# Kernel tuning notes

Measured on AMD Instinct MI355X. Metric: run time of the kernel, lower is better.

The kernel has to match this reference:

```python
import jax, jax.numpy as jnp
from jax import lax
import numpy as np

B, DIM, HEADS, H, W = 4, 384, 8, 128, 128


def conv2d(x, w, b, groups=1, pad=0):
    # x: NCHW, w: OIHW (I = in_channels // groups)
    y = lax.conv_general_dilated(
        x, w, window_strides=(1, 1), padding=[(pad, pad), (pad, pad)],
        dimension_numbers=("NCHW", "OIHW", "NCHW"), feature_group_count=groups)
    return y + b[None, :, None, None]


def _l2norm(x, eps=1e-12):
    # torch F.normalize(dim=-1): x / max(||x||_2, eps)
    n = jnp.sqrt(jnp.sum(x * x, axis=-1, keepdims=True))
    return x / jnp.maximum(n, eps)


def setup_inputs() -> dict:
    key = jax.random.key(0)
    ks = jax.random.split(key, 8)
    s = 0.02
    d = DIM
    return {
        "x": jax.random.normal(ks[0], (B, d, H, W), jnp.float32),
        "feature": jax.random.normal(ks[1], (B, d, H, W), jnp.float32),
        "qkv_w": jax.random.normal(ks[2], (3 * d, d, 1, 1), jnp.float32) * s,
        "qkv_b": jnp.zeros((3 * d,), jnp.float32),
        "dw_w": jax.random.normal(ks[3], (3 * d, 1, 3, 3), jnp.float32) * s,  # depthwise, groups=3d
        "dw_b": jnp.zeros((3 * d,), jnp.float32),
        "qdw_w": jax.random.normal(ks[4], (2 * d, 1, 3, 3), jnp.float32) * s,  # depthwise, groups=2d
        "qdw_b": jnp.zeros((2 * d,), jnp.float32),
        "qpw_w": jax.random.normal(ks[5], (d, 2 * d, 1, 1), jnp.float32) * s,
        "qpw_b": jnp.zeros((d,), jnp.float32),
        "proj_w": jax.random.normal(ks[6], (d, d, 1, 1), jnp.float32) * s,
        "proj_b": jnp.zeros((d,), jnp.float32),
        "temperature": jnp.ones((HEADS, 1, 1), jnp.float32),
        "K": 24,  # top-k count == int(C * 0.5) with C = DIM // HEADS = 48
    }


def reference(x, feature, qkv_w, qkv_b, dw_w, dw_b, qdw_w, qdw_b,
              qpw_w, qpw_b, proj_w, proj_b, temperature, K):
    b, c, h, w = x.shape
    # qkv = dwconv3x3(conv1x1(x))
    qkv = conv2d(conv2d(x, qkv_w, qkv_b), dw_w, dw_b, groups=3 * c, pad=1)
    q, k, v = jnp.split(qkv, 3, axis=1)
    # q branch: dwconv3x3 on cat([q, feature]) -> GELU(exact) -> 1x1 conv
    qf = conv2d(jnp.concatenate([q, feature], axis=1), qdw_w, qdw_b, groups=2 * c, pad=1)
    qf = jax.nn.gelu(qf, approximate=False)
    q = conv2d(qf, qpw_w, qpw_b)

    def heads(t):
        return t.reshape(b, HEADS, c // HEADS, h * w)  # b head C (h w)

    q = _l2norm(heads(q))
    k = _l2norm(heads(k))
    v = heads(v)
    # channel attention: [b,head,C,C]
    attn = jnp.einsum("bhcn,bhdn->bhcd", q, k) * temperature
    vals, idx = lax.top_k(attn, K)
    neg = jnp.full_like(attn, -jnp.inf)
    attn = jnp.put_along_axis(neg, idx, vals, axis=-1, inplace=False)
    attn = jax.nn.softmax(attn, axis=-1)
    out = jnp.einsum("bhcd,bhdn->bhcn", attn, v).reshape(b, c, h, w)
    return conv2d(out, proj_w, proj_b)
```

## Files before the change

### kernel.cpp

```cpp
#include <hip/hip_runtime.h>

using u16 = unsigned short;
typedef __attribute__((ext_vector_type(8))) __bf16 bf16x8;
typedef __attribute__((ext_vector_type(4))) float  f32x4;
typedef __attribute__((ext_vector_type(8))) u16    u16x8;
typedef __attribute__((ext_vector_type(4))) u16    u16x4;

#define NB   4
#define DIM  384
#define NPIX 16384

__device__ __forceinline__ u16 f2bf(float f) {
  return __builtin_bit_cast(u16, (__bf16)f);
}
__device__ __forceinline__ float bf2f(u16 u) {
  return (float)__builtin_bit_cast(__bf16, u);
}
__device__ __forceinline__ void gload16(const void* g, void* l) {
  __builtin_amdgcn_global_load_lds(
      (const __attribute__((address_space(1))) void*)g,
      (__attribute__((address_space(3))) void*)l, 16, 0, 0);
}

__global__ void k_cvt(const float* __restrict__ s, u16* __restrict__ d, int n) {
  int i = blockIdx.x * 256 + threadIdx.x;
  if (i < n) d[i] = f2bf(s[i]);
}
__global__ void k_cvt2(const float* __restrict__ s, u16* __restrict__ hi,
                       u16* __restrict__ lo, int n) {
  int i = blockIdx.x * 256 + threadIdx.x;
  if (i < n) {
    float v = s[i];
    u16 h = f2bf(v);
    hi[i] = h;
    lo[i] = f2bf(v - bf2f(h));
  }
}

__global__ void k_splitx(const float* __restrict__ x, u16* __restrict__ xhi,
                         u16* __restrict__ xlo) {
  __shared__ float tile[32][33];
  int n0 = blockIdx.x * 32, c0 = blockIdx.y * 32, b = blockIdx.z;
  int tj = threadIdx.x & 31, ti = threadIdx.x >> 5;
  const float* xp = x + ((size_t)b * DIM + c0) * NPIX + n0;
  #pragma unroll
  for (int i = ti; i < 32; i += 8) tile[i][tj] = xp[(size_t)i * NPIX + tj];
  __syncthreads();
  const size_t ob = ((size_t)b * NPIX + n0) * DIM + c0;
  #pragma unroll
  for (int j = ti; j < 32; j += 8) {
    float v = tile[tj][j];
    u16 h = f2bf(v);
    xhi[ob + (size_t)j * DIM + tj] = h;
    xlo[ob + (size_t)j * DIM + tj] = f2bf(v - bf2f(h));
  }
}

template<int OUTMODE>
__global__ __launch_bounds__(256, 4)
void k_gemmS(const u16* __restrict__ A, const u16* __restrict__ B,
             void* __restrict__ Out, const float* __restrict__ bias,
             int M, int N, int Kd)
{
  __shared__ u16 lA[128 * 64];
  __shared__ u16 lB[128 * 64];
  const int tid = threadIdx.x, wid = tid >> 6, lane = tid & 63;
  const int GX = gridDim.x, GY = gridDim.y;
  const int W = GX * GY * (int)gridDim.z;
  const int w = blockIdx.x + GX * (blockIdx.y + GY * blockIdx.z);
  const int nw = (w & 7) * (W >> 3) + (w >> 3);
  const int mt = nw % GY;
  const int rest = nw / GY;
  const int ntile = rest % GX;
  const int b = rest / GX;
  const int m0 = mt * 128, n0 = ntile * 128;

  const int srow = lane >> 3;
  const int sslot = (lane & 7) ^ srow;
  const size_t rowA = (size_t)(m0 + wid * 32 + srow) * Kd + sslot * 8;
  const size_t rowB = ((size_t)b * N + n0 + wid * 32 + srow) * Kd + sslot * 8;
  u16* lAw = &lA[(wid * 32) * 64];
  u16* lBw = &lB[(wid * 32) * 64];
  const int wm = (wid & 1) * 64, wn = (wid >> 1) * 64;
  const int cl = lane & 15, rl = lane >> 4;
  const int sxa = cl & 7;

  f32x4 acc[4][4];
  const f32x4 fz = {0.f, 0.f, 0.f, 0.f};
  #pragma unroll
  for (int i = 0; i < 4; ++i)
    #pragma unroll
    for (int j = 0; j < 4; ++j) acc[i][j] = fz;

  const int nk = Kd >> 6;
  for (int kt = 0; kt < nk; ++kt) {
    const u16* Ap = A + rowA + kt * 64;
    const u16* Bp = B + rowB + kt * 64;
    __syncthreads();
    #pragma unroll
    for (int i = 0; i < 4; ++i) {
      gload16(Ap + (size_t)(i * 8) * Kd, lAw + i * 8 * 64);
      gload16(Bp + (size_t)(i * 8) * Kd, lBw + i * 8 * 64);
    }
    __syncthreads();
    #pragma unroll
    for (int ks = 0; ks < 2; ++ks) {
      bf16x8 av[4], bv[4];
      #pragma unroll
      for (int i = 0; i < 4; ++i) {
        av[i] = *(const bf16x8*)&lA[(wm + i * 16 + cl) * 64 + ((ks * 4 + rl) ^ sxa) * 8];
        bv[i] = *(const bf16x8*)&lB[(wn + i * 16 + cl) * 64 + ((ks * 4 + rl) ^ sxa) * 8];
      }
      #pragma unroll
      for (int i = 0; i < 4; ++i)
        #pragma unroll
        for (int j = 0; j < 4; ++j)
          acc[i][j] = __builtin_amdgcn_mfma_f32_16x16x32_bf16(av[i], bv[j], acc[i][j], 0, 0, 0);
    }
  }

  #pragma unroll
  for (int i = 0; i < 4; ++i) {
    #pragma unroll
    for (int j = 0; j < 4; ++j) {
      #pragma unroll
      for (int r = 0; r < 4; ++r) {
        const int m = m0 + wm + i * 16 + rl * 4 + r;
        const int n = n0 + wn + j * 16 + cl;
        const float v = acc[i][j][r] + bias[m];
        const size_t o = ((size_t)b * M + m) * N + n;
        if (OUTMODE == 0) ((float*)Out)[o] = v;
        else ((u16*)Out)[o] = f2bf(v);
      }
    }
  }
}

template<int OUTMODE, bool SSQ>
__global__ __launch_bounds__(256, 4)
void k_gemmP(const u16* __restrict__ Ahi, const u16* __restrict__ Alo,
             const u16* __restrict__ Bhi, const u16* __restrict__ Blo,
             void* __restrict__ Out, u16* __restrict__ OutLo,
             const float* __restrict__ bias, float* __restrict__ ssq,
             int M, int N, int Kd)
{
  __shared__ u16 lA[128 * 64];
  __shared__ u16 lB[128 * 64];
  const int tid = threadIdx.x, wid = tid >> 6, lane = tid & 63;
  const int GX = gridDim.x, GY = gridDim.y;
  const int W = GX * GY * (int)gridDim.z;
  const int w = blockIdx.x + GX * (blockIdx.y + GY * blockIdx.z);
  const int nw = (w & 7) * (W >> 3) + (w >> 3);
  const int mt = nw % GY;
  const int rest = nw / GY;
  const int ntile = rest % GX;
  const int b = rest / GX;
  const int m0 = mt * 128, n0 = ntile * 128;

  const int srow = lane >> 3;
  const int sp = (lane & 7) ^ srow;
  const int scol = (sp & 3) * 8;
  const u16* baseA = (sp < 4) ? Ahi : Alo;
  const u16* baseB = (sp < 4) ? Bhi : Blo;
  const u16* srcA[4];
  const u16* srcB[4];
  #pragma unroll
  for (int i = 0; i < 4; ++i) {
    srcA[i] = baseA + (size_t)(m0 + wid * 32 + i * 8 + srow) * Kd + scol;
    srcB[i] = baseB + ((size_t)b * N + n0 + wid * 32 + i * 8 + srow) * Kd + scol;
  }
  u16* lAw = &lA[(wid * 32) * 64];
  u16* lBw = &lB[(wid * 32) * 64];
  const int wm = (wid & 1) * 64, wn = (wid >> 1) * 64;
  const int cl = lane & 15, rl = lane >> 4;
  const int ph = rl ^ (cl & 7);

  f32x4 acc[4][4];
  const f32x4 fz = {0.f, 0.f, 0.f, 0.f};
  #pragma unroll
  for (int i = 0; i < 4; ++i)
    #pragma unroll
    for (int j = 0; j < 4; ++j) acc[i][j] = fz;

  const int nk = Kd >> 5;
  for (int kt = 0; kt < nk; ++kt) {
    __syncthreads();
    #pragma unroll
    for (int i = 0; i < 4; ++i) {
      gload16(srcA[i] + kt * 32, lAw + i * 8 * 64);
      gload16(srcB[i] + kt * 32, lBw + i * 8 * 64);
    }
    __syncthreads();
    bf16x8 avh[4], bvh[4], avl[4], bvl[4];
    #pragma unroll
    for (int i = 0; i < 4; ++i) {
      avh[i] = *(const bf16x8*)&lA[(wm + i * 16 + cl) * 64 + ph * 8];
      bvh[i] = *(const bf16x8*)&lB[(wn + i * 16 + cl) * 64 + ph * 8];
    }
    #pragma unroll
    for (int i = 0; i < 4; ++i)
      #pragma unroll
      for (int j = 0; j < 4; ++j)
        acc[i][j] = __builtin_amdgcn_mfma_f32_16x16x32_bf16(avh[i], bvh[j], acc[i][j], 0, 0, 0);
    #pragma unroll
    for (int i = 0; i < 4; ++i)
      avl[i] = *(const bf16x8*)&lA[(wm + i * 16 + cl) * 64 + (ph ^ 4) * 8];
    #pragma unroll
    for (int i = 0; i < 4; ++i)
      #pragma unroll
      for (int j = 0; j < 4; ++j)
        acc[i][j] = __builtin_amdgcn_mfma_f32_16x16x32_bf16(avl[i], bvh[j], acc[i][j], 0, 0, 0);
    #pragma unroll
    for (int i = 0; i < 4; ++i)
      bvl[i] = *(const bf16x8*)&lB[(wn + i * 16 + cl) * 64 + (ph ^ 4) * 8];
    #pragma unroll
    for (int i = 0; i < 4; ++i)
      #pragma unroll
      for (int j = 0; j < 4; ++j)
        acc[i][j] = __builtin_amdgcn_mfma_f32_16x16x32_bf16(avh[i], bvl[j], acc[i][j], 0, 0, 0);
  }

  float sq[4][4];
  if (SSQ) {
    #pragma unroll
    for (int i = 0; i < 4; ++i)
      #pragma unroll
      for (int r = 0; r < 4; ++r) sq[i][r] = 0.f;
  }
  #pragma unroll
  for (int i = 0; i < 4; ++i) {
    #pragma unroll
    for (int j = 0; j < 4; ++j) {
      #pragma unroll
      for (int r = 0; r < 4; ++r) {
        const int m = m0 + wm + i * 16 + rl * 4 + r;
        const int n = n0 + wn + j * 16 + cl;
        const float v = acc[i][j][r] + bias[m];
        if (SSQ) sq[i][r] += v * v;
        const size_t o = ((size_t)b * M + m) * N + n;
        if (OUTMODE == 0) ((float*)Out)[o] = v;
        else {
          u16 h = f2bf(v);
          ((u16*)Out)[o] = h;
          OutLo[o] = f2bf(v - bf2f(h));
        }
      }
    }
  }
  if (SSQ) {
    #pragma unroll
    for (int i = 0; i < 4; ++i) {
      #pragma unroll
      for (int r = 0; r < 4; ++r) {
        float s = sq[i][r];
        s += __shfl_xor(s, 1);
        s += __shfl_xor(s, 2);
        s += __shfl_xor(s, 4);
        s += __shfl_xor(s, 8);
        if (cl == 0)
          atomicAdd(&ssq[(size_t)b * M + m0 + wm + i * 16 + rl * 4 + r], s);
      }
    }
  }
}

__device__ __forceinline__ void row_acc_f32(const float* __restrict__ rowp,
    int x0, float w0, float w1, float w2,
    float& o0, float& o1, float& o2, float& o3)
{
  float4 r = *(const float4*)(rowp + x0);
  float lm = __shfl_up(r.w, 1);   if (x0 == 0)   lm = 0.f;
  float rt = __shfl_down(r.x, 1); if (x0 == 124) rt = 0.f;
  o0 = fmaf(lm,  w0, fmaf(r.x, w1, fmaf(r.y, w2, o0)));
  o1 = fmaf(r.x, w0, fmaf(r.y, w1, fmaf(r.z, w2, o1)));
  o2 = fmaf(r.y, w0, fmaf(r.z, w1, fmaf(r.w, w2, o2)));
  o3 = fmaf(r.z, w0, fmaf(r.w, w1, fmaf(rt,  w2, o3)));
}
__device__ __forceinline__ void row_acc_bf16(const u16* __restrict__ rowp,
    int x0, float w0, float w1, float w2,
    float& o0, float& o1, float& o2, float& o3)
{
  u16x4 rv = *(const u16x4*)(rowp + x0);
  float r0 = bf2f(rv[0]), r1 = bf2f(rv[1]), r2 = bf2f(rv[2]), r3 = bf2f(rv[3]);
  float lm = __shfl_up(r3, 1);   if (x0 == 0)   lm = 0.f;
  float rt = __shfl_down(r0, 1); if (x0 == 124) rt = 0.f;
  o0 = fmaf(lm, w0, fmaf(r0, w1, fmaf(r1, w2, o0)));
  o1 = fmaf(r0, w0, fmaf(r1, w1, fmaf(r2, w2, o1)));
  o2 = fmaf(r1, w0, fmaf(r2, w1, fmaf(r3, w2, o2)));
  o3 = fmaf(r2, w0, fmaf(r3, w1, fmaf(rt, w2, o3)));
}

__global__ __launch_bounds__(256, 4)
void k_dw3qk(const float* __restrict__ src, const float* __restrict__ w9,
             const float* __restrict__ bias, float* __restrict__ qdwbuf,
             u16* __restrict__ khi, u16* __restrict__ klo,
             float* __restrict__ ssqk)
{
  const int tid = threadIdx.x, wv = tid >> 6, lane = tid & 63;
  const int n0 = blockIdx.x * 1024 + tid * 4;
  const int h = n0 >> 7, x0 = n0 & 127;
  const int c0 = blockIdx.y * 8, b = blockIdx.z;
  const int hm = (h > 0) ? h - 1 : 0, hp = (h < 127) ? h + 1 : 127;
  const float topf = (h > 0) ? 1.f : 0.f, botf = (h < 127) ? 1.f : 0.f;
  const float* base = src + ((size_t)b * 768 + c0) * NPIX;
  const bool isk = (c0 >= 384);
  float ssl[8];
  #pragma unroll
  for (int s = 0; s < 8; ++s) {
    const int c = c0 + s;
    const float* sp = base + (size_t)s * NPIX;
    const float* wc = w9 + c * 9;
    const float bz = bias[c];
    float o0 = bz, o1 = bz, o2 = bz, o3 = bz;
    row_acc_f32(sp + hm * 128, x0, wc[0] * topf, wc[1] * topf, wc[2] * topf, o0, o1, o2, o3);
    row_acc_f32(sp + h  * 128, x0, wc[3], wc[4], wc[5], o0, o1, o2, o3);
    row_acc_f32(sp + hp * 128, x0, wc[6] * botf, wc[7] * botf, wc[8] * botf, o0, o1, o2, o3);
    if (!isk) {
      float4 ov = make_float4(o0, o1, o2, o3);
      *(float4*)(qdwbuf + ((size_t)b * 384 + c) * NPIX + n0) = ov;
      ssl[s] = 0.f;
    } else {
      ssl[s] = o0 * o0 + o1 * o1 + o2 * o2 + o3 * o3;
      u16x4 ph, pl;
      float oo[4] = {o0, o1, o2, o3};
      #pragma unroll
      for (int j = 0; j < 4; ++j) {
        u16 hv = f2bf(oo[j]);
        ph[j] = hv;
        pl[j] = f2bf(oo[j] - bf2f(hv));
      }
      const size_t off = ((size_t)b * 384 + (c - 384)) * NPIX + n0;
      *(u16x4*)(khi + off) = ph;
      *(u16x4*)(klo + off) = pl;
    }
  }
  if (isk) {
    __shared__ float sred[4][8];
    #pragma unroll
    for (int s = 0; s < 8; ++s) {
      float v = ssl[s];
      #pragma unroll
      for (int off = 32; off; off >>= 1) v += __shfl_down(v, off);
      if (lane == 0) sred[wv][s] = v;
    }
    __syncthreads();
    if (tid < 8) {
      float t = sred[0][tid] + sred[1][tid] + sred[2][tid] + sred[3][tid];
      atomicAdd(&ssqk[(size_t)b * DIM + (c0 - 384) + tid], t);
    }
  }
}

__global__ __launch_bounds__(256, 4)
void k_dw3v(const u16* __restrict__ src, const float* __restrict__ w9,
            const float* __restrict__ bias, u16* __restrict__ vout)
{
  const int tid = threadIdx.x;
  const int n0 = blockIdx.x * 1024 + tid * 4;
  const int h = n0 >> 7, x0 = n0 & 127;
  const int c0 = blockIdx.y * 8, b = blockIdx.z;
  const int hm = (h > 0) ? h - 1 : 0, hp = (h < 127) ? h + 1 : 127;
  const float topf = (h > 0) ? 1.f : 0.f, botf = (h < 127) ? 1.f : 0.f;
  const u16* base = src + ((size_t)b * 384 + c0) * NPIX;
  #pragma unroll
  for (int s = 0; s < 8; ++s) {
    const int c = c0 + s;
    const u16* sp = base + (size_t)s * NPIX;
    const float* wc = w9 + c * 9;
    const float bz = bias[c];
    float o0 = bz, o1 = bz, o2 = bz, o3 = bz;
    row_acc_bf16(sp + hm * 128, x0, wc[0] * topf, wc[1] * topf, wc[2] * topf, o0, o1, o2, o3);
    row_acc_bf16(sp + h  * 128, x0, wc[3], wc[4], wc[5], o0, o1, o2, o3);
    row_acc_bf16(sp + hp * 128, x0, wc[6] * botf, wc[7] * botf, wc[8] * botf, o0, o1, o2, o3);
    u16x4 pk;
    pk[0] = f2bf(o0); pk[1] = f2bf(o1); pk[2] = f2bf(o2); pk[3] = f2bf(o3);
    *(u16x4*)(vout + ((size_t)b * 384 + c) * NPIX + n0) = pk;
  }
}

__global__ __launch_bounds__(512, 4)
void k_qdw2(const float* __restrict__ qdwbuf, const float* __restrict__ feat,
            const float* __restrict__ w9, const float* __restrict__ bias,
            u16* __restrict__ qfhi, u16* __restrict__ qflo)
{
  __shared__ u16 th[256 * 64];
  __shared__ u16 tl[256 * 64];
  const int tid = threadIdx.x, wv = tid >> 6, lane = tid & 63;
  const int whw = blockIdx.x + 64 * (blockIdx.y + 12 * blockIdx.z);
  const int g = (whw & 7) + 8 * (whw >> 9);
  const int xchunk = (whw >> 3) & 63;
  const int cg = g % 12, b = g / 12;
  const int npx0 = xchunk * 256;
  const int n0 = npx0 + lane * 4;
  const int h = n0 >> 7, x0 = n0 & 127;
  const int c0 = cg * 64 + wv * 8;
  const int hm = (h > 0) ? h - 1 : 0, hp = (h < 127) ? h + 1 : 127;
  const float topf = (h > 0) ? 1.f : 0.f, botf = (h < 127) ? 1.f : 0.f;
  const bool isq = (c0 < 384);
  const float* base = isq ? (qdwbuf + ((size_t)b * 384 + c0) * NPIX)
                          : (feat   + ((size_t)b * 384 + (c0 - 384)) * NPIX);
  u16x8 vh[4], vl[4];
  #pragma unroll
  for (int s = 0; s < 8; ++s) {
    const int c = c0 + s;
    const float* sp = base + (size_t)s * NPIX;
    const float* wc = w9 + c * 9;
    const float bz = bias[c];
    float o0 = bz, o1 = bz, o2 = bz, o3 = bz;
    row_acc_f32(sp + hm * 128, x0, wc[0] * topf, wc[1] * topf, wc[2] * topf, o0, o1, o2, o3);
    row_acc_f32(sp + h  * 128, x0, wc[3], wc[4], wc[5], o0, o1, o2, o3);
    row_acc_f32(sp + hp * 128, x0, wc[6] * botf, wc[7] * botf, wc[8] * botf, o0, o1, o2, o3);
    float oo[4] = {o0, o1, o2, o3};
    #pragma unroll
    for (int j = 0; j < 4; ++j) {
      const float a = oo[j];
      const float g2 = 0.5f * a * (1.0f + erff(a * 0.70710678118654752440f));
      const u16 hv = f2bf(g2);
      vh[j][s] = hv;
      vl[j][s] = f2bf(g2 - bf2f(hv));
    }
  }
  const int sl = (wv ^ (lane & 7)) * 8;
  #pragma unroll
  for (int j = 0; j < 4; ++j) {
    const int px = lane * 4 + j;
    *(u16x8*)&th[px * 64 + sl] = vh[j];
    *(u16x8*)&tl[px * 64 + sl] = vl[j];
  }
  __syncthreads();
  const int sel = tid >> 8;
  const int px = tid & 255;
  const u16* srcb = sel ? tl : th;
  u16* dst = (sel ? qflo : qfhi) +
             ((size_t)b * NPIX + npx0 + px) * 768 + cg * 64;
  const int rsw = (px >> 2) & 7;
  #pragma unroll
  for (int s = 0; s < 8; ++s)
    *(u16x8*)(dst + s * 8) = *(const u16x8*)&srcb[px * 64 + ((s ^ rsw) * 8)];
}

__global__ __launch_bounds__(256)
void k_qk3(const u16* __restrict__ qhi, const u16* __restrict__ qlo,
           const u16* __restrict__ khi, const u16* __restrict__ klo,
           float* __restrict__ part)
{
  const int wid = threadIdx.x >> 6, lane = threadIdx.x & 63;
  const int chunk = blockIdx.x, bh = blockIdx.y;
  const int b = bh >> 3, hd = bh & 7;
  const int n0 = chunk * 512 + wid * 128;
  const size_t base = ((size_t)b * 384 + hd * 48) * NPIX;
  const int cl = lane & 15, rl = lane >> 4;
  f32x4 acc[3][3];
  const f32x4 fz = {0.f, 0.f, 0.f, 0.f};
  #pragma unroll
  for (int i = 0; i < 3; ++i)
    #pragma unroll
    for (int j = 0; j < 3; ++j) acc[i][j] = fz;
  #pragma unroll
  for (int ks = 0; ks < 4; ++ks) {
    const int nn = n0 + ks * 32 + rl * 8;
    bf16x8 ah[3], al[3], bh16[3], bl16[3];
    #pragma unroll
    for (int i = 0; i < 3; ++i) {
      const size_t ro = base + (size_t)(i * 16 + cl) * NPIX + nn;
      ah[i]   = *(const bf16x8*)&qhi[ro];
      al[i]   = *(const bf16x8*)&qlo[ro];
      bh16[i] = *(const bf16x8*)&khi[ro];
      bl16[i] = *(const bf16x8*)&klo[ro];
    }
    #pragma unroll
    for (int i = 0; i < 3; ++i)
      #pragma unroll
      for (int j = 0; j < 3; ++j) {
        acc[i][j] = __builtin_amdgcn_mfma_f32_16x16x32_bf16(ah[i], bh16[j], acc[i][j], 0, 0, 0);
        acc[i][j] = __builtin_amdgcn_mfma_f32_16x16x32_bf16(ah[i], bl16[j], acc[i][j], 0, 0, 0);
        acc[i][j] = __builtin_amdgcn_mfma_f32_16x16x32_bf16(al[i], bh16[j], acc[i][j], 0, 0, 0);
      }
  }
  float* pp = part + ((size_t)bh * 128 + chunk * 4 + wid) * 2304;
  #pragma unroll
  for (int i = 0; i < 3; ++i)
    #pragma unroll
    for (int j = 0; j < 3; ++j)
      #pragma unroll
      for (int r = 0; r < 4; ++r)
        pp[(i * 16 + rl * 4 + r) * 48 + (j * 16 + cl)] = acc[i][j][r];
}

__global__ void k_qkred(const float* __restrict__ part, float* __restrict__ raw)
{
  const int bh = blockIdx.x;
  const int p = blockIdx.y * 256 + threadIdx.x;
  const float* pp = part + (size_t)bh * 128 * 2304 + p;
  float s = 0.f;
  #pragma unroll 8
  for (int w = 0; w < 128; ++w) s += pp[(size_t)w * 2304];
  raw[(size_t)bh * 2304 + p] = s;
}

__global__ void k_topk(const float* __restrict__ raw, const float* __restrict__ ssq_q,
                       const float* __restrict__ ssq_k, const float* __restrict__ temp,
                       const int* __restrict__ Kp, float* __restrict__ attn)
{
  const int bh = blockIdx.x, b = bh >> 3, hd = bh & 7;
  const int c = threadIdx.x;
  if (c >= 48) return;
  const int K = *Kp;
  const float qi = temp[hd] / fmaxf(sqrtf(ssq_q[b * DIM + hd * 48 + c]), 1e-12f);
  float vals[48];
  for (int d = 0; d < 48; ++d) {
    const float ki = 1.0f / fmaxf(sqrtf(ssq_k[b * DIM + hd * 48 + d]), 1e-12f);
    vals[d] = raw[(size_t)bh * 2304 + c * 48 + d] * qi * ki;
  }
  float mx = -3.0e38f;
  bool keep[48];
  for (int d = 0; d < 48; ++d) {
    int rank = 0;
    for (int e = 0; e < 48; ++e)
      rank += (vals[e] > vals[d] || (vals[e] == vals[d] && e < d)) ? 1 : 0;
    keep[d] = rank < K;
    if (keep[d]) mx = fmaxf(mx, vals[d]);
  }
  float sum = 0.f;
  for (int d = 0; d < 48; ++d) if (keep[d]) sum += expf(vals[d] - mx);
  const float rs = 1.0f / sum;
  float* ap = attn + (size_t)bh * 2304 + c * 48;
  for (int d = 0; d < 48; ++d) ap[d] = keep[d] ? expf(vals[d] - mx) * rs : 0.f;
}

__global__ __launch_bounds__(256)
void k_pv(const float* __restrict__ attn, const u16* __restrict__ vv, u16* __restrict__ outT)
{
  const int bh = blockIdx.y, b = bh >> 3, hd = bh & 7;
  const int n = blockIdx.x * 256 + threadIdx.x;
  __shared__ float at[2304];
  for (int i = threadIdx.x; i < 2304; i += 256) at[i] = attn[(size_t)bh * 2304 + i];
  __syncthreads();
  const u16* vb = vv + ((size_t)b * 384 + hd * 48) * NPIX + n;
  float acc[48];
  #pragma unroll
  for (int c = 0; c < 48; ++c) acc[c] = 0.f;
  for (int d = 0; d < 48; ++d) {
    const float vvv = bf2f(vb[(size_t)d * NPIX]);
    #pragma unroll
    for (int c = 0; c < 48; ++c) acc[c] += at[c * 48 + d] * vvv;
  }
  u16* dst = outT + ((size_t)b * NPIX + n) * DIM + hd * 48;
  #pragma unroll
  for (int g = 0; g < 6; ++g) {
    u16x8 pk;
    #pragma unroll
    for (int e = 0; e < 8; ++e) pk[e] = f2bf(acc[g * 8 + e]);
    *(u16x8*)(dst + g * 8) = pk;
  }
}

extern "C" void kernel_launch(void* const* d_in, const int* in_sizes, int n_in,
                              void* d_out, int out_size, void* d_ws, size_t ws_size,
                              hipStream_t stream)
{
  (void)in_sizes; (void)n_in; (void)out_size; (void)ws_size;
  const float* x      = (const float*)d_in[0];
  const float* feat   = (const float*)d_in[1];
  const float* qkv_w  = (const float*)d_in[2];
  const float* qkv_b  = (const float*)d_in[3];
  const float* dw_w   = (const float*)d_in[4];
  const float* dw_b   = (const float*)d_in[5];
  const float* qdw_w  = (const float*)d_in[6];
  const float* qdw_b  = (const float*)d_in[7];
  const float* qpw_w  = (const float*)d_in[8];
  const float* qpw_b  = (const float*)d_in[9];
  const float* proj_w = (const float*)d_in[10];
  const float* proj_b = (const float*)d_in[11];
  const float* temp   = (const float*)d_in[12];
  const int*   Kp     = (const int*)d_in[13];

  char* ws = (char*)d_ws;
  const size_t HALF = 50331648;

  u16* WqkvHi = (u16*)ws;
  u16* WqkvLo = WqkvHi + 1152 * 384;
  u16* WqpwHi = WqkvLo + 1152 * 384;
  u16* WqpwLo = WqpwHi + 384 * 768;
  u16* Wproj  = WqpwLo + 384 * 768;
  float* raw  = (float*)(ws + 3244032);
  float* attn = raw + (size_t)32 * 2304;
  float* ssqQ = attn + (size_t)32 * 2304;
  float* ssqK = ssqQ + NB * DIM;
  char* R1 = ws + (16ull << 20);
  u16* xThi = (u16*)R1;
  u16* xTlo = (u16*)(R1 + HALF);
  float* qdwbuf = (float*)R1;
  u16* qHi = (u16*)R1;
  u16* qLo = (u16*)(R1 + HALF);
  u16* vv  = (u16*)R1;
  char* R2 = ws + (112ull << 20);
  float* qkpre = (float*)R2;
  u16* qfHi = (u16*)R2;
  u16* qfLo = (u16*)(R2 + 2 * HALF);
  float* part = (float*)R2;
  u16* aoT  = (u16*)R2;
  u16* vpre = (u16*)(ws + (304ull << 20));
  u16* kHi = (u16*)d_out;
  u16* kLo = kHi + (size_t)NB * DIM * NPIX;

  hipMemsetAsync(ssqQ, 0, 2 * NB * DIM * sizeof(float), stream);
  k_cvt2<<<dim3(1728), 256, 0, stream>>>(qkv_w, WqkvHi, WqkvLo, 1152 * 384);
  k_cvt2<<<dim3(1152), 256, 0, stream>>>(qpw_w, WqpwHi, WqpwLo, 384 * 768);
  k_cvt<<<dim3(576), 256, 0, stream>>>(proj_w, Wproj, 384 * 384);
  k_splitx<<<dim3(512, 12, NB), 256, 0, stream>>>(x, xThi, xTlo);
  k_gemmP<0, false><<<dim3(128, 6, NB), 256, 0, stream>>>(WqkvHi, WqkvLo, xThi, xTlo,
      (void*)qkpre, nullptr, qkv_b, nullptr, 768, NPIX, 384);
  k_gemmS<1><<<dim3(128, 3, NB), 256, 0, stream>>>(WqkvHi + (size_t)768 * 384,
      xThi, (void*)vpre, qkv_b + 768, 384, NPIX, 384);
  k_dw3qk<<<dim3(16, 96, NB), 256, 0, stream>>>(qkpre, dw_w, dw_b, qdwbuf, kHi, kLo, ssqK);
  k_qdw2<<<dim3(64, 12, NB), 512, 0, stream>>>(qdwbuf, feat, qdw_w, qdw_b, qfHi, qfLo);
  k_gemmP<2, true><<<dim3(128, 3, NB), 256, 0, stream>>>(WqpwHi, WqpwLo, qfHi, qfLo,
      (void*)qHi, qLo, qpw_b, ssqQ, 384, NPIX, 768);
  k_qk3<<<dim3(32, 32), 256, 0, stream>>>(qHi, qLo, kHi, kLo, part);
  k_qkred<<<dim3(32, 9), 256, 0, stream>>>(part, raw);
  k_dw3v<<<dim3(16, 48, NB), 256, 0, stream>>>(vpre, dw_w + 768 * 9, dw_b + 768, vv);
  k_topk<<<dim3(32), 64, 0, stream>>>(raw, ssqQ, ssqK, temp, Kp, attn);
  k_pv<<<dim3(64, 32), 256, 0, stream>>>(attn, vv, aoT);
  k_gemmS<0><<<dim3(128, 3, NB), 256, 0, stream>>>(Wproj, aoT,
      d_out, proj_b, 384, NPIX, 384);
}
```

Baseline: 910.1 us.

## Fold attention matrix into projection weights and drop separate PV pass

Instead of computing attn@V per pixel and then projecting, a small kernel precomputes per-batch combined weights proj_w·blockdiag(attn) in bf16. The final GEMM applies them directly to a transposed V, which the depthwise V kernel now writes through an LDS transpose. This removes the k_pv pass and its intermediate buffer traffic. qk3 also handles two chunks per block, halving the partial-sum buffer and the reduction work. The combined weights are rounded once to bf16, which may change accuracy slightly.

```diff
diff --git a/kernel.cpp b/kernel.cpp
--- a/kernel.cpp
+++ b/kernel.cpp
@@ -22,10 +22,6 @@
       (__attribute__((address_space(3))) void*)l, 16, 0, 0);
 }
 
-__global__ void k_cvt(const float* __restrict__ s, u16* __restrict__ d, int n) {
-  int i = blockIdx.x * 256 + threadIdx.x;
-  if (i < n) d[i] = f2bf(s[i]);
-}
 __global__ void k_cvt2(const float* __restrict__ s, u16* __restrict__ hi,
                        u16* __restrict__ lo, int n) {
   int i = blockIdx.x * 256 + threadIdx.x;
@@ -60,7 +56,7 @@
 __global__ __launch_bounds__(256, 4)
 void k_gemmS(const u16* __restrict__ A, const u16* __restrict__ B,
              void* __restrict__ Out, const float* __restrict__ bias,
-             int M, int N, int Kd)
+             int M, int N, int Kd, size_t Astride)
 {
   __shared__ u16 lA[128 * 64];
   __shared__ u16 lB[128 * 64];
@@ -77,7 +73,8 @@
 
   const int srow = lane >> 3;
   const int sslot = (lane & 7) ^ srow;
-  const size_t rowA = (size_t)(m0 + wid * 32 + srow) * Kd + sslot * 8;
+  const size_t rowA = (size_t)(m0 + wid * 32 + srow) * Kd + sslot * 8 +
+                      (size_t)b * Astride;
   const size_t rowB = ((size_t)b * N + n0 + wid * 32 + srow) * Kd + sslot * 8;
   u16* lAw = &lA[(wid * 32) * 64];
   u16* lBw = &lB[(wid * 32) * 64];
@@ -351,17 +348,24 @@
   }
 }
 
-__global__ __launch_bounds__(256, 4)
-void k_dw3v(const u16* __restrict__ src, const float* __restrict__ w9,
-            const float* __restrict__ bias, u16* __restrict__ vout)
-{
-  const int tid = threadIdx.x;
-  const int n0 = blockIdx.x * 1024 + tid * 4;
+__global__ __launch_bounds__(512, 4)
+void k_dw3vT(const u16* __restrict__ src, const float* __restrict__ w9,
+             const float* __restrict__ bias, u16* __restrict__ vT)
+{
+  __shared__ u16 th[256 * 64];
+  const int tid = threadIdx.x, wv = tid >> 6, lane = tid & 63;
+  const int whw = blockIdx.x + 64 * (blockIdx.y + 6 * blockIdx.z);
+  const int g = (whw & 7) + 8 * (whw >> 9);
+  const int xchunk = (whw >> 3) & 63;
+  const int cg = g % 6, b = g / 6;
+  const int npx0 = xchunk * 256;
+  const int n0 = npx0 + lane * 4;
   const int h = n0 >> 7, x0 = n0 & 127;
-  const int c0 = blockIdx.y * 8, b = blockIdx.z;
+  const int c0 = cg * 64 + wv * 8;
   const int hm = (h > 0) ? h - 1 : 0, hp = (h < 127) ? h + 1 : 127;
   const float topf = (h > 0) ? 1.f : 0.f, botf = (h < 127) ? 1.f : 0.f;
   const u16* base = src + ((size_t)b * 384 + c0) * NPIX;
+  u16x8 vh[4];
   #pragma unroll
   for (int s = 0; s < 8; ++s) {
     const int c = c0 + s;
@@ -372,9 +376,23 @@
     row_acc_bf16(sp + hm * 128, x0, wc[0] * topf, wc[1] * topf, wc[2] * topf, o0, o1, o2, o3);
     row_acc_bf16(sp + h  * 128, x0, wc[3], wc[4], wc[5], o0, o1, o2, o3);
     row_acc_bf16(sp + hp * 128, x0, wc[6] * botf, wc[7] * botf, wc[8] * botf, o0, o1, o2, o3);
-    u16x4 pk;
-    pk[0] = f2bf(o0); pk[1] = f2bf(o1); pk[2] = f2bf(o2); pk[3] = f2bf(o3);
-    *(u16x4*)(vout + ((size_t)b * 384 + c) * NPIX + n0) = pk;
+    vh[0][s] = f2bf(o0); vh[1][s] = f2bf(o1);
+    vh[2][s] = f2bf(o2); vh[3][s] = f2bf(o3);
+  }
+  const int sl = (wv ^ (lane & 7)) * 8;
+  #pragma unroll
+  for (int j = 0; j < 4; ++j) {
+    const int px = lane * 4 + j;
+    *(u16x8*)&th[px * 64 + sl] = vh[j];
+  }
+  __syncthreads();
+  if (tid < 256) {
+    const int px = tid;
+    u16* dst = vT + ((size_t)b * NPIX + npx0 + px) * 384 + cg * 64;
+    const int rsw = (px >> 2) & 7;
+    #pragma unroll
+    for (int s = 0; s < 8; ++s)
+      *(u16x8*)(dst + s * 8) = *(const u16x8*)&th[px * 64 + ((s ^ rsw) * 8)];
   }
 }
 
@@ -445,9 +463,8 @@
            float* __restrict__ part)
 {
   const int wid = threadIdx.x >> 6, lane = threadIdx.x & 63;
-  const int chunk = blockIdx.x, bh = blockIdx.y;
+  const int bh = blockIdx.y;
   const int b = bh >> 3, hd = bh & 7;
-  const int n0 = chunk * 512 + wid * 128;
   const size_t base = ((size_t)b * 384 + hd * 48) * NPIX;
   const int cl = lane & 15, rl = lane >> 4;
   f32x4 acc[3][3];
@@ -456,28 +473,31 @@
   for (int i = 0; i < 3; ++i)
     #pragma unroll
     for (int j = 0; j < 3; ++j) acc[i][j] = fz;
-  #pragma unroll
-  for (int ks = 0; ks < 4; ++ks) {
-    const int nn = n0 + ks * 32 + rl * 8;
-    bf16x8 ah[3], al[3], bh16[3], bl16[3];
-    #pragma unroll
-    for (int i = 0; i < 3; ++i) {
-      const size_t ro = base + (size_t)(i * 16 + cl) * NPIX + nn;
-      ah[i]   = *(const bf16x8*)&qhi[ro];
-      al[i]   = *(const bf16x8*)&qlo[ro];
-      bh16[i] = *(const bf16x8*)&khi[ro];
-      bl16[i] = *(const bf16x8*)&klo[ro];
-    }
-    #pragma unroll
-    for (int i = 0; i < 3; ++i)
-      #pragma unroll
-      for (int j = 0; j < 3; ++j) {
-        acc[i][j] = __builtin_amdgcn_mfma_f32_16x16x32_bf16(ah[i], bh16[j], acc[i][j], 0, 0, 0);
-        acc[i][j] = __builtin_amdgcn_mfma_f32_16x16x32_bf16(ah[i], bl16[j], acc[i][j], 0, 0, 0);
-        acc[i][j] = __builtin_amdgcn_mfma_f32_16x16x32_bf16(al[i], bh16[j], acc[i][j], 0, 0, 0);
+  for (int ck = 0; ck < 2; ++ck) {
+    const int n0 = (blockIdx.x * 2 + ck) * 512 + wid * 128;
+    #pragma unroll
+    for (int ks = 0; ks < 4; ++ks) {
+      const int nn = n0 + ks * 32 + rl * 8;
+      bf16x8 ah[3], al[3], bh16[3], bl16[3];
+      #pragma unroll
+      for (int i = 0; i < 3; ++i) {
+        const size_t ro = base + (size_t)(i * 16 + cl) * NPIX + nn;
+        ah[i]   = *(const bf16x8*)&qhi[ro];
+        al[i]   = *(const bf16x8*)&qlo[ro];
+        bh16[i] = *(const bf16x8*)&khi[ro];
+        bl16[i] = *(const bf16x8*)&klo[ro];
       }
-  }
-  float* pp = part + ((size_t)bh * 128 + chunk * 4 + wid) * 2304;
+      #pragma unroll
+      for (int i = 0; i < 3; ++i)
+        #pragma unroll
+        for (int j = 0; j < 3; ++j) {
+          acc[i][j] = __builtin_amdgcn_mfma_f32_16x16x32_bf16(ah[i], bh16[j], acc[i][j], 0, 0, 0);
+          acc[i][j] = __builtin_amdgcn_mfma_f32_16x16x32_bf16(ah[i], bl16[j], acc[i][j], 0, 0, 0);
+          acc[i][j] = __builtin_amdgcn_mfma_f32_16x16x32_bf16(al[i], bh16[j], acc[i][j], 0, 0, 0);
+        }
+    }
+  }
+  float* pp = part + ((size_t)bh * 64 + blockIdx.x * 4 + wid) * 2304;
   #pragma unroll
   for (int i = 0; i < 3; ++i)
     #pragma unroll
@@ -491,10 +511,10 @@
 {
   const int bh = blockIdx.x;
   const int p = blockIdx.y * 256 + threadIdx.x;
-  const float* pp = part + (size_t)bh * 128 * 2304 + p;
+  const float* pp = part + (size_t)bh * 64 * 2304 + p;
   float s = 0.f;
   #pragma unroll 8
-  for (int w = 0; w < 128; ++w) s += pp[(size_t)w * 2304];
+  for (int w = 0; w < 64; ++w) s += pp[(size_t)w * 2304];
   raw[(size_t)bh * 2304 + p] = s;
 }
 
@@ -528,30 +548,20 @@
   for (int d = 0; d < 48; ++d) ap[d] = keep[d] ? expf(vals[d] - mx) * rs : 0.f;
 }
 
-__global__ __launch_bounds__(256)
-void k_pv(const float* __restrict__ attn, const u16* __restrict__ vv, u16* __restrict__ outT)
-{
-  const int bh = blockIdx.y, b = bh >> 3, hd = bh & 7;
-  const int n = blockIdx.x * 256 + threadIdx.x;
+__global__ void k_wa(const float* __restrict__ W, const float* __restrict__ attn,
+                     u16* __restrict__ WaHi)
+{
+  const int bh = blockIdx.x, b = bh >> 3, hd = bh & 7;
   __shared__ float at[2304];
   for (int i = threadIdx.x; i < 2304; i += 256) at[i] = attn[(size_t)bh * 2304 + i];
   __syncthreads();
-  const u16* vb = vv + ((size_t)b * 384 + hd * 48) * NPIX + n;
-  float acc[48];
-  #pragma unroll
-  for (int c = 0; c < 48; ++c) acc[c] = 0.f;
-  for (int d = 0; d < 48; ++d) {
-    const float vvv = bf2f(vb[(size_t)d * NPIX]);
-    #pragma unroll
-    for (int c = 0; c < 48; ++c) acc[c] += at[c * 48 + d] * vvv;
-  }
-  u16* dst = outT + ((size_t)b * NPIX + n) * DIM + hd * 48;
-  #pragma unroll
-  for (int g = 0; g < 6; ++g) {
-    u16x8 pk;
-    #pragma unroll
-    for (int e = 0; e < 8; ++e) pk[e] = f2bf(acc[g * 8 + e]);
-    *(u16x8*)(dst + g * 8) = pk;
+  for (int idx = threadIdx.x; idx < 384 * 48; idx += 256) {
+    const int m = idx / 48, d = idx - m * 48;
+    const float* wr = W + (size_t)m * 384 + hd * 48;
+    float s = 0.f;
+    #pragma unroll
+    for (int c = 0; c < 48; ++c) s += wr[c] * at[c * 48 + d];
+    WaHi[((size_t)b * 384 + m) * 384 + hd * 48 + d] = f2bf(s);
   }
 }
 
@@ -582,24 +592,23 @@
   u16* WqkvLo = WqkvHi + 1152 * 384;
   u16* WqpwHi = WqkvLo + 1152 * 384;
   u16* WqpwLo = WqpwHi + 384 * 768;
-  u16* Wproj  = WqpwLo + 384 * 768;
   float* raw  = (float*)(ws + 3244032);
   float* attn = raw + (size_t)32 * 2304;
   float* ssqQ = attn + (size_t)32 * 2304;
   float* ssqK = ssqQ + NB * DIM;
+  u16* WaHi   = (u16*)(ws + (4ull << 20));
   char* R1 = ws + (16ull << 20);
   u16* xThi = (u16*)R1;
   u16* xTlo = (u16*)(R1 + HALF);
   float* qdwbuf = (float*)R1;
   u16* qHi = (u16*)R1;
   u16* qLo = (u16*)(R1 + HALF);
-  u16* vv  = (u16*)R1;
   char* R2 = ws + (112ull << 20);
   float* qkpre = (float*)R2;
   u16* qfHi = (u16*)R2;
   u16* qfLo = (u16*)(R2 + 2 * HALF);
   float* part = (float*)R2;
-  u16* aoT  = (u16*)R2;
+  u16* vT   = (u16*)R2;
   u16* vpre = (u16*)(ws + (304ull << 20));
   u16* kHi = (u16*)d_out;
   u16* kLo = kHi + (size_t)NB * DIM * NPIX;
@@ -607,21 +616,20 @@
   hipMemsetAsync(ssqQ, 0, 2 * NB * DIM * sizeof(float), stream);
   k_cvt2<<<dim3(1728), 256, 0, stream>>>(qkv_w, WqkvHi, WqkvLo, 1152 * 384);
   k_cvt2<<<dim3(1152), 256, 0, stream>>>(qpw_w, WqpwHi, WqpwLo, 384 * 768);
-  k_cvt<<<dim3(576), 256, 0, stream>>>(proj_w, Wproj, 384 * 384);
   k_splitx<<<dim3(512, 12, NB), 256, 0, stream>>>(x, xThi, xTlo);
   k_gemmP<0, false><<<dim3(128, 6, NB), 256, 0, stream>>>(WqkvHi, WqkvLo, xThi, xTlo,
       (void*)qkpre, nullptr, qkv_b, nullptr, 768, NPIX, 384);
   k_gemmS<1><<<dim3(128, 3, NB), 256, 0, stream>>>(WqkvHi + (size_t)768 * 384,
-      xThi, (void*)vpre, qkv_b + 768, 384, NPIX, 384);
+      xThi, (void*)vpre, qkv_b + 768, 384, NPIX, 384, 0);
   k_dw3qk<<<dim3(16, 96, NB), 256, 0, stream>>>(qkpre, dw_w, dw_b, qdwbuf, kHi, kLo, ssqK);
   k_qdw2<<<dim3(64, 12, NB), 512, 0, stream>>>(qdwbuf, feat, qdw_w, qdw_b, qfHi, qfLo);
   k_gemmP<2, true><<<dim3(128, 3, NB), 256, 0, stream>>>(WqpwHi, WqpwLo, qfHi, qfLo,
       (void*)qHi, qLo, qpw_b, ssqQ, 384, NPIX, 768);
-  k_qk3<<<dim3(32, 32), 256, 0, stream>>>(qHi, qLo, kHi, kLo, part);
+  k_qk3<<<dim3(16, 32), 256, 0, stream>>>(qHi, qLo, kHi, kLo, part);
   k_qkred<<<dim3(32, 9), 256, 0, stream>>>(part, raw);
-  k_dw3v<<<dim3(16, 48, NB), 256, 0, stream>>>(vpre, dw_w + 768 * 9, dw_b + 768, vv);
+  k_dw3vT<<<dim3(64, 6, NB), 512, 0, stream>>>(vpre, dw_w + 768 * 9, dw_b + 768, vT);
   k_topk<<<dim3(32), 64, 0, stream>>>(raw, ssqQ, ssqK, temp, Kp, attn);
-  k_pv<<<dim3(64, 32), 256, 0, stream>>>(attn, vv, aoT);
-  k_gemmS<0><<<dim3(128, 3, NB), 256, 0, stream>>>(Wproj, aoT,
-      d_out, proj_b, 384, NPIX, 384);
-}
+  k_wa<<<dim3(32), 256, 0, stream>>>(proj_w, attn, WaHi);
+  k_gemmS<0><<<dim3(128, 3, NB), 256, 0, stream>>>(WaHi, vT,
+      d_out, proj_b, 384, NPIX, 384, (size_t)384 * 384);
+}
```

Result: no change. 896.4 us (-1.5%).
